# Performance work log

Measured on AMD Instinct MI355X. Metric: run time of the kernel, lower is better.

The kernel has to match this reference:

```python
import jax, jax.numpy as jnp
import numpy as np

N = 100000      # nodes
E = 1000000     # edges per branch
C_IN = 128      # in_channels
C_OUT = 64      # out_channels
BN_EPS = 1e-5


def setup_inputs() -> dict:
    key = jax.random.key(0)
    ks = jax.random.split(key, 8)
    inp = {"x": jax.random.normal(ks[0], (N, C_IN), jnp.float32)}
    for i, name in enumerate(["edge_index_p", "edge_index_s", "edge_index_v"]):
        inp[name] = jax.random.randint(ks[1 + i], (2, E), 0, N, dtype=jnp.int32)
    # input BatchNorm1d affine params
    inp["in_gamma"] = jnp.ones((C_IN,), jnp.float32)
    inp["in_beta"] = jnp.zeros((C_IN,), jnp.float32)
    # per-branch GIN MLP params, stacked over the 3 branches (p, s, v)
    inp["W1"] = jax.random.normal(ks[4], (3, C_IN, C_OUT), jnp.float32) * 0.05
    inp["b1"] = jnp.zeros((3, C_OUT), jnp.float32)
    inp["W2"] = jax.random.normal(ks[5], (3, C_OUT, C_OUT), jnp.float32) * 0.05
    inp["b2"] = jnp.zeros((3, C_OUT), jnp.float32)
    # per-branch output BatchNorm1d affine params
    inp["bn_gamma"] = jnp.ones((3, C_OUT), jnp.float32)
    inp["bn_beta"] = jnp.zeros((3, C_OUT), jnp.float32)
    return inp


def _batchnorm(h, gamma, beta):
    # training-mode BatchNorm1d: batch stats over the node dim, biased variance
    mu = h.mean(axis=0)
    var = ((h - mu) ** 2).mean(axis=0)
    return gamma * (h - mu) * jax.lax.rsqrt(var + BN_EPS) + beta


def reference(x, edge_index_p, edge_index_s, edge_index_v,
              in_gamma, in_beta, W1, b1, W2, b2, bn_gamma, bn_beta):
    n = x.shape[0]
    xn = _batchnorm(x, in_gamma, in_beta)  # in_norm
    outs = []
    for i, ei in enumerate([edge_index_p, edge_index_s, edge_index_v]):
        src, dst = ei[0], ei[1]
        # GINConv (eps=0): sum-aggregate neighbor features, add self
        agg = jax.ops.segment_sum(xn[src], dst, num_segments=n)  # [N, C_IN]
        h = xn + agg
        # MLP([C_IN, C_OUT, C_OUT]) with ReLU between, plain last layer
        h = jax.nn.relu(h @ W1[i] + b1[i])
        h = h @ W2[i] + b2[i]
        # post-GIN BatchNorm1d + Tanh
        outs.append(jnp.tanh(_batchnorm(h, bn_gamma[i], bn_beta[i])))
    return tuple(outs)  # (x_p, x_s, x_v)
```

## Files before the change

kernel.cpp:

```cpp
#include <hip/hip_runtime.h>
#include <math.h>

#define NN   100000
#define NE   1000000
#define CIN  128
#define COUT 64
#define BN_EPS 1e-5f
#define NB    391
#define NBLK1 128
#define CHUNK_E ((NE + NBLK1 - 1) / NBLK1)

#define Y1B_OFF    0
#define COL_OFF    9600000
#define ROWPTR_OFF 12600000
#define OFF_OFF    12900016
#define W1P_OFF    13050160
#define C1_OFF     (W1P_OFF + 3*CIN*COUT)
#define INSUM_OFF  (C1_OFF + 3*COUT)
#define INSQ_OFF   (INSUM_OFF + CIN)
#define OSUM_OFF   (INSQ_OFF + CIN)
#define OSQ_OFF    (OSUM_OFF + 3*COUT)
#define SCALE_OFF  (OSQ_OFF + 3*COUT)
#define SHIFT_OFF  (SCALE_OFF + CIN)
#define OBNS_OFF   (SHIFT_OFF + CIN)
#define OBNB_OFF   (OBNS_OFF + 3*COUT)
#define ZERO_OFF   INSUM_OFF
#define ZERO_CNT   (2*CIN + 6*COUT)

__device__ __forceinline__ unsigned bf16_rne(float f) {
    unsigned u = __float_as_uint(f);
    return (u + 0x7FFFu + ((u >> 16) & 1u)) >> 16;
}
__device__ __forceinline__ float lo16f(unsigned u) { return __uint_as_float(u << 16); }
__device__ __forceinline__ float hi16f(unsigned u) { return __uint_as_float(u & 0xFFFF0000u); }

__global__ __launch_bounds__(256) void k_in_stats(const float* __restrict__ x,
                                                  float* __restrict__ ws) {
    int tid = blockIdx.x * blockDim.x + threadIdx.x;
    int c = tid & (CIN - 1);
    int r0 = tid >> 7;
    int rstride = (gridDim.x * blockDim.x) >> 7;
    float s = 0.f, ss = 0.f;
    for (int r = r0; r < NN; r += rstride) {
        float v = x[(size_t)r * CIN + c];
        s += v; ss += v * v;
    }
    unsafeAtomicAdd(&ws[INSUM_OFF + c], s);
    unsafeAtomicAdd(&ws[INSQ_OFF + c], ss);
}

__global__ void k_in_finalize(const float* __restrict__ g, const float* __restrict__ b,
                              float* __restrict__ ws) {
    int c = threadIdx.x;
    float mu  = ws[INSUM_OFF + c] * (1.f / NN);
    float var = ws[INSQ_OFF + c] * (1.f / NN) - mu * mu;
    float sc  = g[c] * rsqrtf(var + BN_EPS);
    ws[SCALE_OFF + c] = sc;
    ws[SHIFT_OFF + c] = b[c] - mu * sc;
}

__global__ void k_fold(const float* __restrict__ W1, float* __restrict__ ws) {
    int idx = blockIdx.x * blockDim.x + threadIdx.x;
    int k = (idx >> 6) & (CIN - 1);
    ws[W1P_OFF + idx] = ws[SCALE_OFF + k] * W1[idx];
}

__global__ void k_c1(const float* __restrict__ W1, float* __restrict__ ws) {
    int i = blockIdx.x, o = threadIdx.x;
    float acc = 0.f;
    for (int k = 0; k < CIN; ++k)
        acc = fmaf(ws[SHIFT_OFF + k], W1[i * CIN * COUT + k * COUT + o], acc);
    ws[C1_OFF + i * COUT + o] = acc;
}

__global__ __launch_bounds__(256) void k_sort_hist(const int* __restrict__ e0,
                                                   const int* __restrict__ e1,
                                                   const int* __restrict__ e2,
                                                   int* __restrict__ wsi) {
    int z = blockIdx.y;
    const int* ei = (z == 0) ? e0 : (z == 1) ? e1 : e2;
    __shared__ int h[NB];
    for (int i = threadIdx.x; i < NB; i += 256) h[i] = 0;
    __syncthreads();
    int beg = blockIdx.x * CHUNK_E;
    int end = min(NE, beg + CHUNK_E);
    for (int e = beg + threadIdx.x; e < end; e += 256)
        atomicAdd(&h[ei[NE + e] >> 8], 1);
    __syncthreads();
    int* off = wsi + OFF_OFF + z * (NB * NBLK1);
    for (int i = threadIdx.x; i < NB; i += 256)
        off[i * NBLK1 + blockIdx.x] = h[i];
}

__global__ __launch_bounds__(1024) void k_sort_scan(int* __restrict__ wsi) {
    int z = blockIdx.x;
    int* off = wsi + OFF_OFF + z * (NB * NBLK1);
    const int TOT = NB * NBLK1;
    const int CH = (TOT + 1023) / 1024;
    __shared__ int sh[1024];
    int t = threadIdx.x;
    int base = t * CH;
    int s = 0;
    for (int i = 0; i < CH; ++i) {
        int idx = base + i;
        if (idx < TOT) s += off[idx];
    }
    sh[t] = s;
    __syncthreads();
    for (int o = 1; o < 1024; o <<= 1) {
        int v = (t >= o) ? sh[t - o] : 0;
        __syncthreads();
        sh[t] += v;
        __syncthreads();
    }
    int run = sh[t] - s;
    for (int i = 0; i < CH; ++i) {
        int idx = base + i;
        if (idx < TOT) {
            int v = off[idx];
            off[idx] = run;
            run += v;
        }
    }
}

__global__ __launch_bounds__(256) void k_sort_scatter(const int* __restrict__ e0,
                                                      const int* __restrict__ e1,
                                                      const int* __restrict__ e2,
                                                      int* __restrict__ wsi) {
    int z = blockIdx.y;
    const int* ei = (z == 0) ? e0 : (z == 1) ? e1 : e2;
    const int* off = wsi + OFF_OFF + z * (NB * NBLK1);
    unsigned* temp = (unsigned*)wsi + (size_t)z * NE;
    __shared__ int cur[NB];
    for (int i = threadIdx.x; i < NB; i += 256)
        cur[i] = off[i * NBLK1 + blockIdx.x];
    __syncthreads();
    int beg = blockIdx.x * CHUNK_E;
    int end = min(NE, beg + CHUNK_E);
    for (int e = beg + threadIdx.x; e < end; e += 256) {
        int d = ei[NE + e];
        int s = ei[e];
        int pos = atomicAdd(&cur[d >> 8], 1);
        temp[pos] = ((unsigned)(d & 255) << 24) | (unsigned)s;
    }
}

__global__ __launch_bounds__(256) void k_bucket(int* __restrict__ wsi) {
    int z = blockIdx.y, bk = blockIdx.x;
    const int* off = wsi + OFF_OFF + z * (NB * NBLK1);
    const unsigned* temp = (const unsigned*)wsi + (size_t)z * NE;
    int* col    = wsi + COL_OFF + z * NE;
    int* rowptr = wsi + ROWPTR_OFF + z * (NN + 1);
    int bs = off[bk * NBLK1];
    int be = (bk + 1 < NB) ? off[(bk + 1) * NBLK1] : NE;
    __shared__ int h[256], sc[256], cur[256];
    int t = threadIdx.x;
    h[t] = 0;
    __syncthreads();
    for (int e = bs + t; e < be; e += 256)
        atomicAdd(&h[temp[e] >> 24], 1);
    __syncthreads();
    int v = h[t];
    sc[t] = v;
    __syncthreads();
    for (int o = 1; o < 256; o <<= 1) {
        int u = (t >= o) ? sc[t - o] : 0;
        __syncthreads();
        sc[t] += u;
        __syncthreads();
    }
    int excl = sc[t] - v;
    int gd = bk * 256 + t;
    if (gd <= NN) rowptr[gd] = bs + excl;
    cur[t] = excl;
    __syncthreads();
    for (int e = bs + t; e < be; e += 256) {
        unsigned p = temp[e];
        int pos = atomicAdd(&cur[p >> 24], 1);
        col[bs + pos] = (int)(p & 0x00FFFFFFu);
    }
}

__global__ __launch_bounds__(256, 2) void k_gemm1(const float* __restrict__ x,
                                                  const float* __restrict__ W1p_all,
                                                  const float* __restrict__ c1_all,
                                                  unsigned* __restrict__ y1b_all) {
    int lane = threadIdx.x & 63;
    int wave = (blockIdx.x * blockDim.x + threadIdx.x) >> 6;
    int nw   = (gridDim.x * blockDim.x) >> 6;
    float c1v0 = c1_all[lane];
    float c1v1 = c1_all[COUT + lane];
    float c1v2 = c1_all[2 * COUT + lane];
    const int NGRP = NN / 8;
    for (int g = wave; g < NGRP; g += nw) {
        int n0 = __builtin_amdgcn_readfirstlane(g) * 8;
        const float* __restrict__ xr = x + (size_t)n0 * CIN;
        float a0[8], a1[8], a2[8];
        #pragma unroll
        for (int i = 0; i < 8; ++i) { a0[i] = c1v0; a1[i] = c1v1; a2[i] = c1v2; }
        #pragma unroll 1
        for (int kc = 0; kc < CIN; kc += 16) {
            float w0[16], w1[16], w2[16];
            #pragma unroll
            for (int j = 0; j < 16; ++j) {
                w0[j] = W1p_all[(kc + j) * COUT + lane];
                w1[j] = W1p_all[CIN * COUT + (kc + j) * COUT + lane];
                w2[j] = W1p_all[2 * CIN * COUT + (kc + j) * COUT + lane];
            }
            #pragma unroll
            for (int i = 0; i < 8; ++i) {
                #pragma unroll
                for (int j = 0; j < 16; ++j) {
                    float xv = xr[i * CIN + kc + j];
                    a0[i] = fmaf(xv, w0[j], a0[i]);
                    a1[i] = fmaf(xv, w1[j], a1[i]);
                    a2[i] = fmaf(xv, w2[j], a2[i]);
                }
            }
        }
        #define STORE_NODE(zz, az, i) { \
            float vhi_ = __shfl(az[i], (lane & 31) + 32); \
            if (lane < 32) { \
                unsigned wrd_ = bf16_rne(az[i]) | (bf16_rne(vhi_) << 16); \
                y1b_all[((size_t)(zz) * NN + n0 + (i)) * 32 + lane] = wrd_; \
            } }
        #pragma unroll
        for (int i = 0; i < 8; ++i) {
            STORE_NODE(0, a0, i)
            STORE_NODE(1, a1, i)
            STORE_NODE(2, a2, i)
        }
        #undef STORE_NODE
    }
}

__global__ __launch_bounds__(256) void k_gather(const float* __restrict__ b1all,
                                                float* __restrict__ tall,
                                                float* __restrict__ ws) {
    int z = blockIdx.y;
    const unsigned* __restrict__ y1b = (const unsigned*)ws + Y1B_OFF + (size_t)z * NN * 32;
    float* __restrict__ t = tall + (size_t)z * NN * COUT;
    const int* __restrict__ rowptr = (const int*)ws + ROWPTR_OFF + z * (NN + 1);
    const int* __restrict__ col    = (const int*)ws + COL_OFF + z * NE;
    int lane = threadIdx.x & 63;
    int w32  = lane & 31;
    int half = lane >> 5;
    float b1lo = b1all[z * COUT + w32];
    float b1hi = b1all[z * COUT + 32 + w32];
    int wave = (blockIdx.x * blockDim.x + threadIdx.x) >> 6;
    int nw   = (gridDim.x * blockDim.x) >> 6;
    const int NP = NN / 2;
    for (int p = wave; p < NP; p += nw) {
        int n = p * 2 + half;
        int beg = rowptr[n], end = rowptr[n + 1];
        unsigned su = y1b[(size_t)n * 32 + w32];
        float alo = lo16f(su), ahi = hi16f(su);
        float blo = 0.f, bhi = 0.f, clo = 0.f, chi = 0.f, dlo = 0.f, dhi = 0.f;
        int j = beg;
        for (; j + 3 < end; j += 4) {
            int c0 = col[j], c1 = col[j + 1], c2 = col[j + 2], c3 = col[j + 3];
            unsigned u0 = y1b[(size_t)c0 * 32 + w32];
            unsigned u1 = y1b[(size_t)c1 * 32 + w32];
            unsigned u2 = y1b[(size_t)c2 * 32 + w32];
            unsigned u3 = y1b[(size_t)c3 * 32 + w32];
            alo += lo16f(u0); ahi += hi16f(u0);
            blo += lo16f(u1); bhi += hi16f(u1);
            clo += lo16f(u2); chi += hi16f(u2);
            dlo += lo16f(u3); dhi += hi16f(u3);
        }
        for (; j < end; ++j) {
            unsigned u = y1b[(size_t)col[j] * 32 + w32];
            alo += lo16f(u); ahi += hi16f(u);
        }
        t[(size_t)n * 64 + w32]      = fmaxf((alo + blo) + (clo + dlo) + b1lo, 0.f);
        t[(size_t)n * 64 + 32 + w32] = fmaxf((ahi + bhi) + (chi + dhi) + b1hi, 0.f);
    }
}

__global__ __launch_bounds__(256) void k_mlp2(const float* __restrict__ W2all,
                                              const float* __restrict__ b2all,
                                              float* __restrict__ outall) {
    int z = blockIdx.y;
    const float* __restrict__ W2 = W2all + z * COUT * COUT;
    const float* __restrict__ b2 = b2all + z * COUT;
    float* __restrict__ out = outall + (size_t)z * NN * COUT;
    int lane = threadIdx.x & 63;
    int wave = (blockIdx.x * blockDim.x + threadIdx.x) >> 6;
    int nw   = (gridDim.x * blockDim.x) >> 6;
    const int NTL = (NN + 63) / 64;
    for (int tl = wave; tl < NTL; tl += nw) {
        int n = tl * 64 + lane;
        int nc = (n < NN) ? n : NN - 1;
        bool valid = (n < NN);
        const float4* __restrict__ tr = (const float4*)(out + (size_t)nc * COUT);
        float4 T0 = tr[0],  T1 = tr[1],  T2 = tr[2],  T3 = tr[3];
        float4 T4 = tr[4],  T5 = tr[5],  T6 = tr[6],  T7 = tr[7];
        float4 T8 = tr[8],  T9 = tr[9],  T10 = tr[10], T11 = tr[11];
        float4 T12 = tr[12], T13 = tr[13], T14 = tr[14], T15 = tr[15];
        float4* __restrict__ ow = (float4*)(out + (size_t)nc * COUT);
        #pragma unroll 1
        for (int p = 0; p < 4; ++p) {
            const float* __restrict__ w2p = W2 + p * 16;
            float acc[16];
            #pragma unroll
            for (int o = 0; o < 16; ++o) acc[o] = b2[p * 16 + o];
#define FMA16(tj, jj) { float tjv_ = (tj); \
            _Pragma("unroll") \
            for (int o = 0; o < 16; ++o) \
                acc[o] = fmaf(tjv_, w2p[(jj) * COUT + o], acc[o]); }
#define DO4(Tv, jb) FMA16(Tv.x, 4*(jb)) FMA16(Tv.y, 4*(jb)+1) \
                    FMA16(Tv.z, 4*(jb)+2) FMA16(Tv.w, 4*(jb)+3)
            DO4(T0, 0)  DO4(T1, 1)  DO4(T2, 2)  DO4(T3, 3)
            DO4(T4, 4)  DO4(T5, 5)  DO4(T6, 6)  DO4(T7, 7)
            DO4(T8, 8)  DO4(T9, 9)  DO4(T10, 10) DO4(T11, 11)
            DO4(T12, 12) DO4(T13, 13) DO4(T14, 14) DO4(T15, 15)
#undef DO4
#undef FMA16
            if (valid) {
                ow[p * 4 + 0] = make_float4(acc[0], acc[1], acc[2], acc[3]);
                ow[p * 4 + 1] = make_float4(acc[4], acc[5], acc[6], acc[7]);
                ow[p * 4 + 2] = make_float4(acc[8], acc[9], acc[10], acc[11]);
                ow[p * 4 + 3] = make_float4(acc[12], acc[13], acc[14], acc[15]);
            }
        }
    }
}

__global__ __launch_bounds__(256) void k_h2_stats(const float* __restrict__ outall,
                                                  float* __restrict__ ws) {
    int z = blockIdx.y;
    const float* __restrict__ h = outall + (size_t)z * NN * COUT;
    int tid = blockIdx.x * blockDim.x + threadIdx.x;
    int o = tid & 63;
    int r0 = tid >> 6;
    int rs = (gridDim.x * blockDim.x) >> 6;
    float s = 0.f, ss = 0.f;
    for (int r = r0; r < NN; r += rs) {
        float v = h[(size_t)r * COUT + o];
        s += v; ss += v * v;
    }
    unsafeAtomicAdd(&ws[OSUM_OFF + z * COUT + o], s);
    unsafeAtomicAdd(&ws[OSQ_OFF + z * COUT + o], ss);
}

__global__ void k_obn_final(const float* __restrict__ g, const float* __restrict__ b,
                            float* __restrict__ ws) {
    int br = blockIdx.x;
    int o = threadIdx.x;
    float mu  = ws[OSUM_OFF + br * COUT + o] * (1.f / NN);
    float var = ws[OSQ_OFF  + br * COUT + o] * (1.f / NN) - mu * mu;
    float sc  = g[br * COUT + o] * rsqrtf(var + BN_EPS);
    ws[OBNS_OFF + br * COUT + o] = sc;
    ws[OBNB_OFF + br * COUT + o] = b[br * COUT + o] - mu * sc;
}

__global__ __launch_bounds__(256) void k_apply(float* __restrict__ outall,
                                               const float* __restrict__ ws) {
    int z = blockIdx.y;
    float* out = outall + (size_t)z * NN * COUT;
    const float* __restrict__ sc = ws + OBNS_OFF + z * COUT;
    const float* __restrict__ sh = ws + OBNB_OFF + z * COUT;
    int idx = blockIdx.x * blockDim.x + threadIdx.x;
    int stride = gridDim.x * blockDim.x;
    const int total = NN * COUT / 4;
    float4* o4 = (float4*)out;
    for (int v = idx; v < total; v += stride) {
        int c = (v & 15) * 4;
        float4 f = o4[v];
        f.x = tanhf(fmaf(f.x, sc[c],     sh[c]));
        f.y = tanhf(fmaf(f.y, sc[c + 1], sh[c + 1]));
        f.z = tanhf(fmaf(f.z, sc[c + 2], sh[c + 2]));
        f.w = tanhf(fmaf(f.w, sc[c + 3], sh[c + 3]));
        o4[v] = f;
    }
}

extern "C" void kernel_launch(void* const* d_in, const int* in_sizes, int n_in,
                              void* d_out, int out_size, void* d_ws, size_t ws_size,
                              hipStream_t stream) {
    const float* x   = (const float*)d_in[0];
    const int*   eip = (const int*)d_in[1];
    const int*   eis = (const int*)d_in[2];
    const int*   eiv = (const int*)d_in[3];
    const float* ig  = (const float*)d_in[4];
    const float* ib  = (const float*)d_in[5];
    const float* W1  = (const float*)d_in[6];
    const float* b1  = (const float*)d_in[7];
    const float* W2  = (const float*)d_in[8];
    const float* b2  = (const float*)d_in[9];
    const float* bng = (const float*)d_in[10];
    const float* bnb = (const float*)d_in[11];
    float* out = (float*)d_out;
    float* ws  = (float*)d_ws;
    int*   wsi = (int*)d_ws;

    hipMemsetAsync(ws + ZERO_OFF, 0, ZERO_CNT * sizeof(float), stream);

    k_in_stats<<<256, 256, 0, stream>>>(x, ws);
    k_in_finalize<<<1, 128, 0, stream>>>(ig, ib, ws);
    k_fold<<<96, 256, 0, stream>>>(W1, ws);
    k_c1<<<3, 64, 0, stream>>>(W1, ws);

    k_sort_hist<<<dim3(NBLK1, 3), 256, 0, stream>>>(eip, eis, eiv, wsi);
    k_sort_scan<<<3, 1024, 0, stream>>>(wsi);
    k_sort_scatter<<<dim3(NBLK1, 3), 256, 0, stream>>>(eip, eis, eiv, wsi);
    k_bucket<<<dim3(NB, 3), 256, 0, stream>>>(wsi);

    k_gemm1<<<1024, 256, 0, stream>>>(x, ws + W1P_OFF, ws + C1_OFF,
                                      (unsigned*)ws + Y1B_OFF);
    k_gather<<<dim3(2048, 3), 256, 0, stream>>>(b1, out, ws);
    k_mlp2<<<dim3(391, 3), 256, 0, stream>>>(W2, b2, out);
    k_h2_stats<<<dim3(256, 3), 256, 0, stream>>>(out, ws);
    k_obn_final<<<3, 64, 0, stream>>>(bng, bnb, ws);
    k_apply<<<dim3(1024, 3), 256, 0, stream>>>(out, ws);
}
```

Before: 564.5 us.

## Fuse output BatchNorm statistics into second MLP layer with lane-per-channel mapping

Restructures k_mlp2 so each wave handles 8 consecutive nodes and each lane owns one output channel. W2 columns are held in registers and the input rows are read as wave-uniform broadcast loads. The per-channel sum and sum-of-squares are accumulated in registers and atomically added at the end, which removes the separate k_h2_stats pass over the output. The kernel now reads and writes the same buffer in place, which is safe only because each wave finishes all reads of its rows before writing them. Each tile now depends on scalar or broadcast loads of t instead of per-lane vector loads.

```diff
diff --git a/kernel.cpp b/kernel.cpp
--- a/kernel.cpp
+++ b/kernel.cpp
@@ -280,68 +280,47 @@
 
 __global__ __launch_bounds__(256) void k_mlp2(const float* __restrict__ W2all,
                                               const float* __restrict__ b2all,
-                                              float* __restrict__ outall) {
+                                              const float* __restrict__ tall,
+                                              float* outall,
+                                              float* __restrict__ ws) {
     int z = blockIdx.y;
     const float* __restrict__ W2 = W2all + z * COUT * COUT;
-    const float* __restrict__ b2 = b2all + z * COUT;
-    float* __restrict__ out = outall + (size_t)z * NN * COUT;
+    const float* __restrict__ t = tall + (size_t)z * NN * COUT;
+    float* out = outall + (size_t)z * NN * COUT;
     int lane = threadIdx.x & 63;
     int wave = (blockIdx.x * blockDim.x + threadIdx.x) >> 6;
     int nw   = (gridDim.x * blockDim.x) >> 6;
-    const int NTL = (NN + 63) / 64;
-    for (int tl = wave; tl < NTL; tl += nw) {
-        int n = tl * 64 + lane;
-        int nc = (n < NN) ? n : NN - 1;
-        bool valid = (n < NN);
-        const float4* __restrict__ tr = (const float4*)(out + (size_t)nc * COUT);
-        float4 T0 = tr[0],  T1 = tr[1],  T2 = tr[2],  T3 = tr[3];
-        float4 T4 = tr[4],  T5 = tr[5],  T6 = tr[6],  T7 = tr[7];
-        float4 T8 = tr[8],  T9 = tr[9],  T10 = tr[10], T11 = tr[11];
-        float4 T12 = tr[12], T13 = tr[13], T14 = tr[14], T15 = tr[15];
-        float4* __restrict__ ow = (float4*)(out + (size_t)nc * COUT);
+    float b2v = b2all[z * COUT + lane];
+    float ls = 0.f, lss = 0.f;
+    const int NGRP = NN / 8;
+    for (int g = wave; g < NGRP; g += nw) {
+        int n0 = __builtin_amdgcn_readfirstlane(g) * 8;
+        const float* __restrict__ tr = t + (size_t)n0 * COUT;
+        float a[8];
+        #pragma unroll
+        for (int i = 0; i < 8; ++i) a[i] = b2v;
         #pragma unroll 1
-        for (int p = 0; p < 4; ++p) {
-            const float* __restrict__ w2p = W2 + p * 16;
-            float acc[16];
+        for (int kc = 0; kc < COUT; kc += 16) {
+            float w[16];
             #pragma unroll
-            for (int o = 0; o < 16; ++o) acc[o] = b2[p * 16 + o];
-#define FMA16(tj, jj) { float tjv_ = (tj); \
-            _Pragma("unroll") \
-            for (int o = 0; o < 16; ++o) \
-                acc[o] = fmaf(tjv_, w2p[(jj) * COUT + o], acc[o]); }
-#define DO4(Tv, jb) FMA16(Tv.x, 4*(jb)) FMA16(Tv.y, 4*(jb)+1) \
-                    FMA16(Tv.z, 4*(jb)+2) FMA16(Tv.w, 4*(jb)+3)
-            DO4(T0, 0)  DO4(T1, 1)  DO4(T2, 2)  DO4(T3, 3)
-            DO4(T4, 4)  DO4(T5, 5)  DO4(T6, 6)  DO4(T7, 7)
-            DO4(T8, 8)  DO4(T9, 9)  DO4(T10, 10) DO4(T11, 11)
-            DO4(T12, 12) DO4(T13, 13) DO4(T14, 14) DO4(T15, 15)
-#undef DO4
-#undef FMA16
-            if (valid) {
-                ow[p * 4 + 0] = make_float4(acc[0], acc[1], acc[2], acc[3]);
-                ow[p * 4 + 1] = make_float4(acc[4], acc[5], acc[6], acc[7]);
-                ow[p * 4 + 2] = make_float4(acc[8], acc[9], acc[10], acc[11]);
-                ow[p * 4 + 3] = make_float4(acc[12], acc[13], acc[14], acc[15]);
+            for (int j = 0; j < 16; ++j)
+                w[j] = W2[(kc + j) * COUT + lane];
+            #pragma unroll
+            for (int i = 0; i < 8; ++i) {
+                #pragma unroll
+                for (int j = 0; j < 16; ++j)
+                    a[i] = fmaf(tr[i * COUT + kc + j], w[j], a[i]);
             }
         }
-    }
-}
-
-__global__ __launch_bounds__(256) void k_h2_stats(const float* __restrict__ outall,
-                                                  float* __restrict__ ws) {
-    int z = blockIdx.y;
-    const float* __restrict__ h = outall + (size_t)z * NN * COUT;
-    int tid = blockIdx.x * blockDim.x + threadIdx.x;
-    int o = tid & 63;
-    int r0 = tid >> 6;
-    int rs = (gridDim.x * blockDim.x) >> 6;
-    float s = 0.f, ss = 0.f;
-    for (int r = r0; r < NN; r += rs) {
-        float v = h[(size_t)r * COUT + o];
-        s += v; ss += v * v;
-    }
-    unsafeAtomicAdd(&ws[OSUM_OFF + z * COUT + o], s);
-    unsafeAtomicAdd(&ws[OSQ_OFF + z * COUT + o], ss);
+        #pragma unroll
+        for (int i = 0; i < 8; ++i) {
+            out[(size_t)(n0 + i) * COUT + lane] = a[i];
+            ls += a[i];
+            lss += a[i] * a[i];
+        }
+    }
+    unsafeAtomicAdd(&ws[OSUM_OFF + z * COUT + lane], ls);
+    unsafeAtomicAdd(&ws[OSQ_OFF + z * COUT + lane], lss);
 }
 
 __global__ void k_obn_final(const float* __restrict__ g, const float* __restrict__ b,
@@ -410,8 +389,7 @@
     k_gemm1<<<1024, 256, 0, stream>>>(x, ws + W1P_OFF, ws + C1_OFF,
                                       (unsigned*)ws + Y1B_OFF);
     k_gather<<<dim3(2048, 3), 256, 0, stream>>>(b1, out, ws);
-    k_mlp2<<<dim3(391, 3), 256, 0, stream>>>(W2, b2, out);
-    k_h2_stats<<<dim3(256, 3), 256, 0, stream>>>(out, ws);
+    k_mlp2<<<dim3(512, 3), 256, 0, stream>>>(W2, b2, out, out, ws);
     k_obn_final<<<3, 64, 0, stream>>>(bng, bnb, ws);
     k_apply<<<dim3(1024, 3), 256, 0, stream>>>(out, ws);
 }
```

Measured after the change: 572.5 us. No clear change (+1.4%).

## Widen gather to uint2 per lane and stage MLP2 tiles through LDS

Applied to the files above, without the earlier changes.

The gather kernel now handles four nodes per wavefront with 16 lanes each, loading 8-byte uint2 (four bf16 values) per lane instead of 4-byte words. This raises memory-level parallelism per edge and makes the output stores float2. The second-layer MLP kernel now stages each 64-node tile through padded shared memory, so global loads and stores are coalesced float4 accesses rather than per-lane strided rows. The cost is extra LDS traffic and a smaller 128-thread block.

```diff
diff --git a/kernel.cpp b/kernel.cpp
--- a/kernel.cpp
+++ b/kernel.cpp
@@ -9,6 +9,8 @@
 #define NB    391
 #define NBLK1 128
 #define CHUNK_E ((NE + NBLK1 - 1) / NBLK1)
+#define MT    64
+#define MG    ((NN + MT - 1) / MT)
 
 #define Y1B_OFF    0
 #define COL_OFF    9600000
@@ -239,91 +241,115 @@
                                                 float* __restrict__ tall,
                                                 float* __restrict__ ws) {
     int z = blockIdx.y;
-    const unsigned* __restrict__ y1b = (const unsigned*)ws + Y1B_OFF + (size_t)z * NN * 32;
+    const uint2* __restrict__ y2 =
+        (const uint2*)((const unsigned*)ws + Y1B_OFF + (size_t)z * NN * 32);
     float* __restrict__ t = tall + (size_t)z * NN * COUT;
     const int* __restrict__ rowptr = (const int*)ws + ROWPTR_OFF + z * (NN + 1);
     const int* __restrict__ col    = (const int*)ws + COL_OFF + z * NE;
     int lane = threadIdx.x & 63;
-    int w32  = lane & 31;
-    int half = lane >> 5;
-    float b1lo = b1all[z * COUT + w32];
-    float b1hi = b1all[z * COUT + 32 + w32];
+    int q = lane & 15;
+    int quarter = lane >> 4;
+    float b1a = b1all[z * COUT + 2 * q];
+    float b1b = b1all[z * COUT + 2 * q + 1];
+    float b1c = b1all[z * COUT + 32 + 2 * q];
+    float b1d = b1all[z * COUT + 33 + 2 * q];
     int wave = (blockIdx.x * blockDim.x + threadIdx.x) >> 6;
     int nw   = (gridDim.x * blockDim.x) >> 6;
-    const int NP = NN / 2;
-    for (int p = wave; p < NP; p += nw) {
-        int n = p * 2 + half;
+    const int NG = NN / 4;
+    for (int g = wave; g < NG; g += nw) {
+        int n = g * 4 + quarter;
         int beg = rowptr[n], end = rowptr[n + 1];
-        unsigned su = y1b[(size_t)n * 32 + w32];
-        float alo = lo16f(su), ahi = hi16f(su);
-        float blo = 0.f, bhi = 0.f, clo = 0.f, chi = 0.f, dlo = 0.f, dhi = 0.f;
+        uint2 su = y2[(size_t)n * 16 + q];
+        float aa = lo16f(su.x), ab = hi16f(su.x);
+        float ac = lo16f(su.y), ad = hi16f(su.y);
+        float ba = 0.f, bb = 0.f, bc = 0.f, bd = 0.f;
+        float ca = 0.f, cb = 0.f, cc = 0.f, cd = 0.f;
+        float da = 0.f, db = 0.f, dc = 0.f, dd = 0.f;
         int j = beg;
         for (; j + 3 < end; j += 4) {
             int c0 = col[j], c1 = col[j + 1], c2 = col[j + 2], c3 = col[j + 3];
-            unsigned u0 = y1b[(size_t)c0 * 32 + w32];
-            unsigned u1 = y1b[(size_t)c1 * 32 + w32];
-            unsigned u2 = y1b[(size_t)c2 * 32 + w32];
-            unsigned u3 = y1b[(size_t)c3 * 32 + w32];
-            alo += lo16f(u0); ahi += hi16f(u0);
-            blo += lo16f(u1); bhi += hi16f(u1);
-            clo += lo16f(u2); chi += hi16f(u2);
-            dlo += lo16f(u3); dhi += hi16f(u3);
+            uint2 u0 = y2[(size_t)c0 * 16 + q];
+            uint2 u1 = y2[(size_t)c1 * 16 + q];
+            uint2 u2 = y2[(size_t)c2 * 16 + q];
+            uint2 u3 = y2[(size_t)c3 * 16 + q];
+            aa += lo16f(u0.x); ab += hi16f(u0.x); ac += lo16f(u0.y); ad += hi16f(u0.y);
+            ba += lo16f(u1.x); bb += hi16f(u1.x); bc += lo16f(u1.y); bd += hi16f(u1.y);
+            ca += lo16f(u2.x); cb += hi16f(u2.x); cc += lo16f(u2.y); cd += hi16f(u2.y);
+            da += lo16f(u3.x); db += hi16f(u3.x); dc += lo16f(u3.y); dd += hi16f(u3.y);
         }
         for (; j < end; ++j) {
-            unsigned u = y1b[(size_t)col[j] * 32 + w32];
-            alo += lo16f(u); ahi += hi16f(u);
+            uint2 u = y2[(size_t)col[j] * 16 + q];
+            aa += lo16f(u.x); ab += hi16f(u.x); ac += lo16f(u.y); ad += hi16f(u.y);
         }
-        t[(size_t)n * 64 + w32]      = fmaxf((alo + blo) + (clo + dlo) + b1lo, 0.f);
-        t[(size_t)n * 64 + 32 + w32] = fmaxf((ahi + bhi) + (chi + dhi) + b1hi, 0.f);
-    }
-}
-
-__global__ __launch_bounds__(256) void k_mlp2(const float* __restrict__ W2all,
+        float2 lo = make_float2(fmaxf((aa + ba) + (ca + da) + b1a, 0.f),
+                                fmaxf((ac + bc) + (cc + dc) + b1b, 0.f));
+        float2 hi = make_float2(fmaxf((ab + bb) + (cb + db) + b1c, 0.f),
+                                fmaxf((ad + bd) + (cd + dd) + b1d, 0.f));
+        *(float2*)(t + (size_t)n * 64 + 2 * q)      = lo;
+        *(float2*)(t + (size_t)n * 64 + 32 + 2 * q) = hi;
+    }
+}
+
+__global__ __launch_bounds__(128) void k_mlp2(const float* __restrict__ W2all,
                                               const float* __restrict__ b2all,
                                               float* __restrict__ outall) {
     int z = blockIdx.y;
+    __shared__ float ts[2][MT][68];
     const float* __restrict__ W2 = W2all + z * COUT * COUT;
     const float* __restrict__ b2 = b2all + z * COUT;
     float* __restrict__ out = outall + (size_t)z * NN * COUT;
     int lane = threadIdx.x & 63;
-    int wave = (blockIdx.x * blockDim.x + threadIdx.x) >> 6;
-    int nw   = (gridDim.x * blockDim.x) >> 6;
-    const int NTL = (NN + 63) / 64;
-    for (int tl = wave; tl < NTL; tl += nw) {
-        int n = tl * 64 + lane;
-        int nc = (n < NN) ? n : NN - 1;
-        bool valid = (n < NN);
-        const float4* __restrict__ tr = (const float4*)(out + (size_t)nc * COUT);
-        float4 T0 = tr[0],  T1 = tr[1],  T2 = tr[2],  T3 = tr[3];
-        float4 T4 = tr[4],  T5 = tr[5],  T6 = tr[6],  T7 = tr[7];
-        float4 T8 = tr[8],  T9 = tr[9],  T10 = tr[10], T11 = tr[11];
-        float4 T12 = tr[12], T13 = tr[13], T14 = tr[14], T15 = tr[15];
-        float4* __restrict__ ow = (float4*)(out + (size_t)nc * COUT);
-        #pragma unroll 1
-        for (int p = 0; p < 4; ++p) {
-            const float* __restrict__ w2p = W2 + p * 16;
-            float acc[16];
-            #pragma unroll
-            for (int o = 0; o < 16; ++o) acc[o] = b2[p * 16 + o];
-#define FMA16(tj, jj) { float tjv_ = (tj); \
-            _Pragma("unroll") \
-            for (int o = 0; o < 16; ++o) \
-                acc[o] = fmaf(tjv_, w2p[(jj) * COUT + o], acc[o]); }
+    int wv = threadIdx.x >> 6;
+    int grp = blockIdx.x * 2 + wv;
+    if (grp >= MG) return;
+    float (*T)[68] = ts[wv];
+    #pragma unroll
+    for (int it = 0; it < 16; ++it) {
+        int f = it * 64 + lane;
+        int nd = f >> 4, jq = f & 15;
+        int ng = grp * MT + nd;
+        if (ng > NN - 1) ng = NN - 1;
+        float4 v = *(const float4*)(out + (size_t)ng * COUT + jq * 4);
+        *(float4*)&T[nd][jq * 4] = v;
+    }
+    float4 T0 = *(float4*)&T[lane][0],  T1 = *(float4*)&T[lane][4];
+    float4 T2 = *(float4*)&T[lane][8],  T3 = *(float4*)&T[lane][12];
+    float4 T4 = *(float4*)&T[lane][16], T5 = *(float4*)&T[lane][20];
+    float4 T6 = *(float4*)&T[lane][24], T7 = *(float4*)&T[lane][28];
+    float4 T8 = *(float4*)&T[lane][32], T9 = *(float4*)&T[lane][36];
+    float4 T10 = *(float4*)&T[lane][40], T11 = *(float4*)&T[lane][44];
+    float4 T12 = *(float4*)&T[lane][48], T13 = *(float4*)&T[lane][52];
+    float4 T14 = *(float4*)&T[lane][56], T15 = *(float4*)&T[lane][60];
+    #pragma unroll 1
+    for (int p = 0; p < 4; ++p) {
+        const float* __restrict__ w2p = W2 + p * 16;
+        float acc[16];
+        #pragma unroll
+        for (int o = 0; o < 16; ++o) acc[o] = b2[p * 16 + o];
+#define FMA16(tv, jj) { float tv_ = (tv); \
+        _Pragma("unroll") \
+        for (int o = 0; o < 16; ++o) \
+            acc[o] = fmaf(tv_, w2p[(jj) * COUT + o], acc[o]); }
 #define DO4(Tv, jb) FMA16(Tv.x, 4*(jb)) FMA16(Tv.y, 4*(jb)+1) \
                     FMA16(Tv.z, 4*(jb)+2) FMA16(Tv.w, 4*(jb)+3)
-            DO4(T0, 0)  DO4(T1, 1)  DO4(T2, 2)  DO4(T3, 3)
-            DO4(T4, 4)  DO4(T5, 5)  DO4(T6, 6)  DO4(T7, 7)
-            DO4(T8, 8)  DO4(T9, 9)  DO4(T10, 10) DO4(T11, 11)
-            DO4(T12, 12) DO4(T13, 13) DO4(T14, 14) DO4(T15, 15)
+        DO4(T0, 0)  DO4(T1, 1)  DO4(T2, 2)  DO4(T3, 3)
+        DO4(T4, 4)  DO4(T5, 5)  DO4(T6, 6)  DO4(T7, 7)
+        DO4(T8, 8)  DO4(T9, 9)  DO4(T10, 10) DO4(T11, 11)
+        DO4(T12, 12) DO4(T13, 13) DO4(T14, 14) DO4(T15, 15)
 #undef DO4
 #undef FMA16
-            if (valid) {
-                ow[p * 4 + 0] = make_float4(acc[0], acc[1], acc[2], acc[3]);
-                ow[p * 4 + 1] = make_float4(acc[4], acc[5], acc[6], acc[7]);
-                ow[p * 4 + 2] = make_float4(acc[8], acc[9], acc[10], acc[11]);
-                ow[p * 4 + 3] = make_float4(acc[12], acc[13], acc[14], acc[15]);
-            }
-        }
+        *(float4*)&T[lane][p * 16 + 0]  = make_float4(acc[0], acc[1], acc[2], acc[3]);
+        *(float4*)&T[lane][p * 16 + 4]  = make_float4(acc[4], acc[5], acc[6], acc[7]);
+        *(float4*)&T[lane][p * 16 + 8]  = make_float4(acc[8], acc[9], acc[10], acc[11]);
+        *(float4*)&T[lane][p * 16 + 12] = make_float4(acc[12], acc[13], acc[14], acc[15]);
+    }
+    #pragma unroll
+    for (int it = 0; it < 16; ++it) {
+        int f = it * 64 + lane;
+        int nd = f >> 4, jq = f & 15;
+        int ng = grp * MT + nd;
+        if (ng < NN)
+            *(float4*)(out + (size_t)ng * COUT + jq * 4) = *(float4*)&T[nd][jq * 4];
     }
 }
 
@@ -410,7 +436,7 @@
     k_gemm1<<<1024, 256, 0, stream>>>(x, ws + W1P_OFF, ws + C1_OFF,
                                       (unsigned*)ws + Y1B_OFF);
     k_gather<<<dim3(2048, 3), 256, 0, stream>>>(b1, out, ws);
-    k_mlp2<<<dim3(391, 3), 256, 0, stream>>>(W2, b2, out);
+    k_mlp2<<<dim3((MG + 1) / 2, 3), 128, 0, stream>>>(W2, b2, out);
     k_h2_stats<<<dim3(256, 3), 256, 0, stream>>>(out, ws);
     k_obn_final<<<3, 64, 0, stream>>>(bng, bnb, ws);
     k_apply<<<dim3(1024, 3), 256, 0, stream>>>(out, ws);
```

Measured after the change: 546.8 us. -3.1%, faster.
